# Performance work log

Hardware: AMD Instinct MI355X
Metric: run time of the kernel (lower is better)

Reference implementation:

```python
import jax, jax.numpy as jnp
import numpy as np

HID = 1024
PRED_LEN = 96


def lstm_cell(x, h, c, Wih, Whh, bih, bhh):
    # PyTorch LSTMCell: gates ordered i, f, g, o
    gates = x @ Wih.T + h @ Whh.T + bih + bhh
    i, f, g, o = jnp.split(gates, 4, axis=-1)
    c_new = jax.nn.sigmoid(f) * c + jax.nn.sigmoid(i) * jnp.tanh(g)
    h_new = jax.nn.sigmoid(o) * jnp.tanh(c_new)
    return h_new, c_new


def time_enc(idx, embs):
    # sum of 4 embedding lookups -> [..., time_encode_dim]
    return sum(e[idx[..., k]] for k, e in enumerate(embs))


def setup_inputs() -> dict:
    key = jax.random.key(0)
    ks = jax.random.split(key, 32)
    B, T, IN, OUT, H, TE = 256, 128, 7, 7, HID, 3
    d = {}
    d["x"] = jax.random.normal(ks[0], (B, T, IN), jnp.float32)
    d["y"] = jax.random.normal(ks[1], (B, PRED_LEN, OUT), jnp.float32)
    d["x_time_encode"] = jax.random.randint(ks[2], (B, T, 4), 0, 7)
    d["y_time_encode"] = jax.random.randint(ks[3], (B, PRED_LEN, 4), 0, 7)
    sizes = (12, 31, 24, 7)
    for i, n in enumerate(sizes):
        d[f"emb{i}"] = jax.random.normal(ks[4 + i], (n, TE), jnp.float32)
    ins = (IN + TE, H, H)
    s = float(1.0 / np.sqrt(H))
    for l in range(3):
        d[f"Wih{l}"] = jax.random.uniform(ks[8 + 4 * l], (4 * H, ins[l]), jnp.float32, -s, s)
        d[f"Whh{l}"] = jax.random.uniform(ks[9 + 4 * l], (4 * H, H), jnp.float32, -s, s)
        d[f"bih{l}"] = jax.random.uniform(ks[10 + 4 * l], (4 * H,), jnp.float32, -s, s)
        d[f"bhh{l}"] = jax.random.uniform(ks[11 + 4 * l], (4 * H,), jnp.float32, -s, s)
    d["fcW"] = jax.random.uniform(ks[20], (OUT, H), jnp.float32, -s, s)
    d["fcb"] = jax.random.uniform(ks[21], (OUT,), jnp.float32, -s, s)
    return d


def reference(x, y, x_time_encode, y_time_encode, emb0, emb1, emb2, emb3,
              Wih0, Whh0, bih0, bhh0, Wih1, Whh1, bih1, bhh1,
              Wih2, Whh2, bih2, bhh2, fcW, fcb):
    embs = (emb0, emb1, emb2, emb3)
    layers = ((Wih0, Whh0, bih0, bhh0),
              (Wih1, Whh1, bih1, bhh1),
              (Wih2, Whh2, bih2, bhh2))
    B = x.shape[0]
    H = Whh0.shape[1]

    # encode: concat time embedding, run stacked LSTM over time (dropout_rate=0 -> no-op)
    xin = jnp.concatenate([x, time_enc(x_time_encode, embs)], axis=-1)  # [B,T,in+te]
    h0 = tuple(jnp.zeros((B, H), x.dtype) for _ in range(3))

    def run_layers(hs, cs, inp):
        nh, nc = [], []
        for l, (Wih, Whh, bih, bhh) in enumerate(layers):
            h, c = lstm_cell(inp, hs[l], cs[l], Wih, Whh, bih, bhh)
            nh.append(h)
            nc.append(c)
            inp = h
        return tuple(nh), tuple(nc)

    def enc_step(carry, xt):
        hs, cs = carry
        hs, cs = run_layers(hs, cs, xt)
        return (hs, cs), None

    (hs, cs), _ = jax.lax.scan(enc_step, (h0, h0), xin.swapaxes(0, 1))

    y0 = hs[-1] @ fcW.T + fcb  # [B, out]

    def dec_step(carry, te_idx):
        hs, cs, y_prev = carry
        inp = jnp.concatenate([y_prev, time_enc(te_idx, embs)], axis=-1)
        hs, cs = run_layers(hs, cs, inp)
        yt = hs[-1] @ fcW.T + fcb
        return (hs, cs, yt), yt

    _, ys = jax.lax.scan(dec_step, (hs, cs, y0),
                         y_time_encode[:, :PRED_LEN - 1].swapaxes(0, 1))
    # [B, predict_len, out]
    return jnp.concatenate([y0[:, None], ys.swapaxes(0, 1)], axis=1)
```

## Files before the change

kernel.cpp:

```cpp
#include <hip/hip_runtime.h>

#define HID   1024
#define BATCH 256
#define TSEQ  128
#define PRED  96
#define IND   7
#define OUTD  7
#define SK    10

typedef __attribute__((ext_vector_type(8))) _Float16 f16x8;
typedef __attribute__((ext_vector_type(4))) float    f32x4;

#define BM   64
#define BN   64
#define GSTR 68

__device__ __forceinline__ float sigmoidf_fast(float x) {
  return 1.0f / (1.0f + __expf(-x));
}
__device__ __forceinline__ float tanhf_fast(float x) {
  float ax = fabsf(x);
  float e  = __expf(-2.0f * ax);
  float r  = (1.0f - e) / (1.0f + e);
  return copysignf(r, x);
}

__device__ __forceinline__ void async_cp16(const void* g, void* l) {
  __builtin_amdgcn_global_load_lds(
      (const __attribute__((address_space(1))) void*)g,
      (__attribute__((address_space(3))) void*)l, 16, 0, 0);
}

#define WBAR(N) asm volatile("s_waitcnt vmcnt(" #N ")\n\ts_barrier" ::: "memory")
#define BARO()  asm volatile("s_barrier" ::: "memory")

__global__ __launch_bounds__(256) void prep_kernel(
    const float* __restrict__ Wih0, const float* __restrict__ Whh0,
    const float* __restrict__ bih0, const float* __restrict__ bhh0,
    const float* __restrict__ Wih1, const float* __restrict__ Whh1,
    const float* __restrict__ bih1, const float* __restrict__ bhh1,
    const float* __restrict__ Wih2, const float* __restrict__ Whh2,
    const float* __restrict__ bih2, const float* __restrict__ bhh2,
    _Float16* __restrict__ B0, _Float16* __restrict__ B1, _Float16* __restrict__ B2,
    float* __restrict__ W0p, float* __restrict__ biasP)
{
  size_t e = (size_t)blockIdx.x * 256 + threadIdx.x;
  const size_t S0 = (size_t)4096 * 1024;
  const size_t S1 = (size_t)4096 * 2048;
  if (e < S0) {
    int n = (int)(e >> 10), k = (int)(e & 1023);
    int nb = n >> 6, gate = (n >> 4) & 3, u = n & 15;
    int r = gate * 1024 + nb * 16 + u;
    B0[e] = (_Float16)Whh0[(size_t)r * 1024 + k];
  } else if (e < S0 + S1) {
    size_t q = e - S0;
    int n = (int)(q >> 11), k = (int)(q & 2047);
    int nb = n >> 6, gate = (n >> 4) & 3, u = n & 15;
    int r = gate * 1024 + nb * 16 + u;
    float v = (k < 1024) ? Wih1[(size_t)r * 1024 + k]
                         : Whh1[(size_t)r * 1024 + (k - 1024)];
    B1[q] = (_Float16)v;
  } else if (e < S0 + 2 * S1) {
    size_t q = e - S0 - S1;
    int n = (int)(q >> 11), k = (int)(q & 2047);
    int nb = n >> 6, gate = (n >> 4) & 3, u = n & 15;
    int r = gate * 1024 + nb * 16 + u;
    float v = (k < 1024) ? Wih2[(size_t)r * 1024 + k]
                         : Whh2[(size_t)r * 1024 + (k - 1024)];
    B2[q] = (_Float16)v;
  } else if (e < S0 + 2 * S1 + 40960) {
    int q = (int)(e - S0 - 2 * S1);
    int n = q / 10, k = q - n * 10;
    int nb = n >> 6, gate = (n >> 4) & 3, u = n & 15;
    int r = gate * 1024 + nb * 16 + u;
    W0p[q] = Wih0[(size_t)r * 10 + k];
  } else if (e < S0 + 2 * S1 + 40960 + 12288) {
    int q = (int)(e - S0 - 2 * S1 - 40960);
    int l = q >> 12, n = q & 4095;
    int nb = n >> 6, gate = (n >> 4) & 3, u = n & 15;
    int r = gate * 1024 + nb * 16 + u;
    const float* bi = (l == 0) ? bih0 : (l == 1) ? bih1 : bih2;
    const float* bh = (l == 0) ? bhh0 : (l == 1) ? bhh1 : bhh2;
    biasP[q] = bi[r] + bh[r];
  }
}

__global__ __launch_bounds__(256) void lstm_wave(
    int d,
    _Float16* __restrict__ h0p0, _Float16* __restrict__ h0p1,
    _Float16* __restrict__ h1p0, _Float16* __restrict__ h1p1,
    _Float16* __restrict__ h2p0, _Float16* __restrict__ h2p1,
    const _Float16* __restrict__ B0g, const _Float16* __restrict__ B1g,
    const _Float16* __restrict__ B2g,
    const float* __restrict__ biasP, const float* __restrict__ W0p,
    float* __restrict__ c0, float* __restrict__ c1, float* __restrict__ c2,
    const float* __restrict__ x, const int* __restrict__ xte,
    const float* __restrict__ e0, const float* __restrict__ e1,
    const float* __restrict__ e2, const float* __restrict__ e3)
{
  __shared__ __align__(16) char smem[32768];
  __shared__ float SmallIn[BM * SK];
  __shared__ float W0s[BN * 11];

  const int layer = blockIdx.y >> 2;
  const int mb = blockIdx.y & 3, nb = blockIdx.x;
  const int t = d - layer;
  if (t < 0 || t >= TSEQ) return;
  const int p = d & 1;

  const _Float16 *A1, *A2; _Float16* ho; const _Float16* Bm;
  const float* bias; float* cst; int Kdim;
  if (layer == 0) {
    A1 = p ? h0p1 : h0p0; A2 = A1;              ho = p ? h0p0 : h0p1;
    Bm = B0g; bias = biasP;        cst = c0; Kdim = 1024;
  } else if (layer == 1) {
    A1 = p ? h0p1 : h0p0; A2 = p ? h1p1 : h1p0; ho = p ? h1p0 : h1p1;
    Bm = B1g; bias = biasP + 4096; cst = c1; Kdim = 2048;
  } else {
    A1 = p ? h1p1 : h1p0; A2 = p ? h2p1 : h2p0; ho = p ? h2p0 : h2p1;
    Bm = B2g; bias = biasP + 8192; cst = c2; Kdim = 2048;
  }
  const int Mbase = mb * BM;
  const int tid = threadIdx.x;

  if (layer == 0 && tid < BM) {
    int Mg = Mbase + tid;
    float v[SK];
    const float* xp = x + ((size_t)Mg * TSEQ + t) * IND;
#pragma unroll
    for (int i = 0; i < IND; ++i) v[i] = xp[i];
    const int* ip = xte + ((size_t)Mg * TSEQ + t) * 4;
    int i0 = ip[0], i1 = ip[1], i2 = ip[2], i3 = ip[3];
#pragma unroll
    for (int dd = 0; dd < 3; ++dd)
      v[IND + dd] = e0[i0 * 3 + dd] + e1[i1 * 3 + dd] + e2[i2 * 3 + dd] + e3[i3 * 3 + dd];
#pragma unroll
    for (int i = 0; i < SK; ++i) SmallIn[tid * SK + i] = v[i];
    const float* wp = W0p + (size_t)(nb * BN + tid) * SK;
#pragma unroll
    for (int i = 0; i < SK; ++i) W0s[tid * 11 + i] = wp[i];
  }

  _Float16* As = (_Float16*)smem;
  _Float16* Bs = (_Float16*)(smem + 16384);

  const int w = tid >> 6, lane = tid & 63;
  const int quad = lane >> 4, l16 = lane & 15;
  const int dr = lane >> 4, ds = lane & 15;

  size_t a_goff[4], b_goff[4];
  int lds_off[4];
#pragma unroll
  for (int i = 0; i < 4; ++i) {
    int lrow = w * 16 + i * 4 + dr;
    int sg = ds ^ (i * 4 + dr);
    a_goff[i] = (size_t)(Mbase + lrow) * (HID * 2) + (size_t)sg * 16;
    b_goff[i] = (size_t)(nb * BN + lrow) * ((size_t)Kdim * 2) + (size_t)sg * 16;
    lds_off[i] = lrow * 256 + ds * 16;
  }

  f32x4 acc[4] = {};

  for (int kk = 0; kk < Kdim; kk += 128) {
    const char* Abase = (kk < 1024)
        ? ((const char*)A1 + (size_t)kk * 2)
        : ((const char*)A2 + (size_t)(kk - 1024) * 2);
    const char* Bbase = (const char*)Bm + (size_t)kk * 2;
#pragma unroll
    for (int i = 0; i < 4; ++i) {
      async_cp16(Abase + a_goff[i], smem + lds_off[i]);
      async_cp16(Bbase + b_goff[i], smem + 16384 + lds_off[i]);
    }
    __syncthreads();
#pragma unroll
    for (int ks = 0; ks < 4; ++ks) {
      int segq = (ks * 4 + quad) ^ l16;
      f16x8 bf = *reinterpret_cast<const f16x8*>(Bs + (w * 16 + l16) * 128 + segq * 8);
#pragma unroll
      for (int mt = 0; mt < 4; ++mt) {
        f16x8 af = *reinterpret_cast<const f16x8*>(As + (mt * 16 + l16) * 128 + segq * 8);
        acc[mt] = __builtin_amdgcn_mfma_f32_16x16x32_f16(af, bf, acc[mt], 0, 0, 0);
      }
    }
    __syncthreads();
  }

  float* Gs = (float*)smem;
#pragma unroll
  for (int mt = 0; mt < 4; ++mt) {
    int row = mt * 16 + quad * 4;
    int col = w * 16 + l16;
#pragma unroll
    for (int r = 0; r < 4; ++r)
      Gs[(row + r) * GSTR + col] = acc[mt][r];
  }
  __syncthreads();

#pragma unroll
  for (int i = 0; i < 4; ++i) {
    int m = (tid >> 4) + i * 16;
    int u = tid & 15;
    float gi = Gs[m * GSTR + u];
    float gf = Gs[m * GSTR + 16 + u];
    float gg = Gs[m * GSTR + 32 + u];
    float go = Gs[m * GSTR + 48 + u];
    int nbase = nb * BN;
    gi += bias[nbase + u];
    gf += bias[nbase + 16 + u];
    gg += bias[nbase + 32 + u];
    go += bias[nbase + 48 + u];
    if (layer == 0) {
#pragma unroll
      for (int k = 0; k < SK; ++k) {
        float sv = SmallIn[m * SK + k];
        gi += sv * W0s[u * 11 + k];
        gf += sv * W0s[(16 + u) * 11 + k];
        gg += sv * W0s[(32 + u) * 11 + k];
        go += sv * W0s[(48 + u) * 11 + k];
      }
    }
    size_t cidx = (size_t)(Mbase + m) * HID + (size_t)nb * 16 + u;
    float cold = cst[cidx];
    float cn = sigmoidf_fast(gf) * cold + sigmoidf_fast(gi) * tanhf_fast(gg);
    float hn = sigmoidf_fast(go) * tanhf_fast(cn);
    cst[cidx] = cn;
    ho[cidx] = (_Float16)hn;
  }
}

template<int KCH, int MODE>
__global__ __launch_bounds__(256) void lstm_pipe(
    int s,
    const _Float16* __restrict__ A1, const _Float16* __restrict__ A2,
    const _Float16* __restrict__ Bm, const float* __restrict__ biasL,
    const float* __restrict__ W0p,
    float* __restrict__ cst, _Float16* __restrict__ hout,
    float* __restrict__ out, const int* __restrict__ yte,
    const float* __restrict__ e0, const float* __restrict__ e1,
    const float* __restrict__ e2, const float* __restrict__ e3,
    const float* __restrict__ fcW, const float* __restrict__ fcb)
{
  __shared__ __align__(16) char smem[3 * 16384];
  __shared__ float SmallIn[BM * SK];
  __shared__ float W0s[BN * 11];

  const int tid = threadIdx.x;
  const int nb = blockIdx.x, mb = blockIdx.y;
  const int Mbase = mb * BM;

  if (MODE == 1 && tid < BM) {
    int Mg = Mbase + tid;
    float v[SK];
    const float* yp = out + (size_t)Mg * (PRED * OUTD) + s * OUTD;
#pragma unroll
    for (int i = 0; i < OUTD; ++i) v[i] = yp[i];
    const int* ip = yte + ((size_t)Mg * PRED + s) * 4;
    int i0 = ip[0], i1 = ip[1], i2 = ip[2], i3 = ip[3];
#pragma unroll
    for (int dd = 0; dd < 3; ++dd)
      v[IND + dd] = e0[i0 * 3 + dd] + e1[i1 * 3 + dd] + e2[i2 * 3 + dd] + e3[i3 * 3 + dd];
#pragma unroll
    for (int i = 0; i < SK; ++i) SmallIn[tid * SK + i] = v[i];
    const float* wp = W0p + (size_t)(nb * BN + tid) * SK;
#pragma unroll
    for (int i = 0; i < SK; ++i) W0s[tid * 11 + i] = wp[i];
  }

  const int w = tid >> 6, lane = tid & 63;
  const int quad = lane >> 4, l16 = lane & 15;
  const int dr = lane >> 3, ds = lane & 7;

  size_t a_goff[2], b_goff[2];
  int lds_off[2];
#pragma unroll
  for (int i = 0; i < 2; ++i) {
    int lrow = w * 16 + i * 8 + dr;
    int sg = ds ^ dr;
    a_goff[i] = (size_t)(Mbase + lrow) * (HID * 2) + (size_t)sg * 16;
    b_goff[i] = (size_t)(nb * BN + lrow) * ((size_t)KCH * 128) + (size_t)sg * 16;
    lds_off[i] = lrow * 128 + ds * 16;
  }

  f32x4 acc[4] = {};

  __syncthreads();

#define ISSUE(c) do { \
    const char* Ab_ = (KCH == 16 || (c) < 16) \
        ? ((const char*)A1 + (size_t)(c) * 128) \
        : ((const char*)A2 + (size_t)((c) - 16) * 128); \
    const char* Bb_ = (const char*)Bm + (size_t)(c) * 128; \
    char* Lb_ = smem + ((c) % 3) * 16384; \
    _Pragma("unroll") \
    for (int i_ = 0; i_ < 2; ++i_) { \
      async_cp16(Ab_ + a_goff[i_], Lb_ + lds_off[i_]); \
      async_cp16(Bb_ + b_goff[i_], Lb_ + 8192 + lds_off[i_]); \
    } } while (0)

  ISSUE(0);
  ISSUE(1);
#pragma unroll
  for (int c = 0; c < KCH; ++c) {
    if (c + 2 < KCH) { ISSUE(c + 2); WBAR(8); }
    else if (c + 2 == KCH) { WBAR(4); }
    else { WBAR(0); }
    {
      const _Float16* As = (const _Float16*)(smem + (c % 3) * 16384);
      const _Float16* Bs = As + 4096;
#pragma unroll
      for (int ks = 0; ks < 2; ++ks) {
        int g = ks * 4 + quad;
        int sp = g ^ (l16 & 7);
        f16x8 bf = *reinterpret_cast<const f16x8*>(Bs + (w * 16 + l16) * 64 + sp * 8);
#pragma unroll
        for (int mt = 0; mt < 4; ++mt) {
          f16x8 af = *reinterpret_cast<const f16x8*>(As + (mt * 16 + l16) * 64 + sp * 8);
          acc[mt] = __builtin_amdgcn_mfma_f32_16x16x32_f16(af, bf, acc[mt], 0, 0, 0);
        }
      }
    }
    BARO();
  }
#undef ISSUE

  __syncthreads();
  float* Gs = (float*)smem;
#pragma unroll
  for (int mt = 0; mt < 4; ++mt) {
    int row = mt * 16 + quad * 4;
    int col = w * 16 + l16;
#pragma unroll
    for (int r = 0; r < 4; ++r)
      Gs[(row + r) * GSTR + col] = acc[mt][r];
  }
  __syncthreads();

  float w7[OUTD];
  if (MODE == 3) {
#pragma unroll
    for (int o = 0; o < OUTD; ++o)
      w7[o] = fcW[(size_t)o * HID + nb * 16 + (tid & 15)];
  }

#pragma unroll
  for (int i = 0; i < 4; ++i) {
    int m = (tid >> 4) + i * 16;
    int u = tid & 15;
    float gi = Gs[m * GSTR + u];
    float gf = Gs[m * GSTR + 16 + u];
    float gg = Gs[m * GSTR + 32 + u];
    float go = Gs[m * GSTR + 48 + u];
    int nbase = nb * BN;
    gi += biasL[nbase + u];
    gf += biasL[nbase + 16 + u];
    gg += biasL[nbase + 32 + u];
    go += biasL[nbase + 48 + u];
    if (MODE == 1) {
#pragma unroll
      for (int k = 0; k < SK; ++k) {
        float sv = SmallIn[m * SK + k];
        gi += sv * W0s[u * 11 + k];
        gf += sv * W0s[(16 + u) * 11 + k];
        gg += sv * W0s[(32 + u) * 11 + k];
        go += sv * W0s[(48 + u) * 11 + k];
      }
    }
    size_t cidx = (size_t)(Mbase + m) * HID + (size_t)nb * 16 + u;
    float cold = cst[cidx];
    float cn = sigmoidf_fast(gf) * cold + sigmoidf_fast(gi) * tanhf_fast(gg);
    float hn = sigmoidf_fast(go) * tanhf_fast(cn);
    cst[cidx] = cn;
    hout[cidx] = (_Float16)hn;

    if (MODE == 3) {
#pragma unroll
      for (int o = 0; o < OUTD; ++o) {
        float r = hn * w7[o];
        r += __shfl_xor(r, 1, 16);
        r += __shfl_xor(r, 2, 16);
        r += __shfl_xor(r, 4, 16);
        r += __shfl_xor(r, 8, 16);
        if (u == 0) {
          float val = r + ((nb == 0) ? fcb[o] : 0.0f);
          atomicAdd(&out[(size_t)(Mbase + m) * (PRED * OUTD) + (s + 1) * OUTD + o], val);
        }
      }
    }
  }
}

__global__ __launch_bounds__(256) void fc_kernel(
    const _Float16* __restrict__ h2, const float* __restrict__ fcW,
    const float* __restrict__ fcb, float* __restrict__ out)
{
  int wv = threadIdx.x >> 6, lane = threadIdx.x & 63;
  int row = blockIdx.x * 4 + wv;
  const _Float16* hp = h2 + (size_t)row * HID + lane * 16;
  float hv[16];
#pragma unroll
  for (int i = 0; i < 16; ++i) hv[i] = (float)hp[i];
  float acc[OUTD];
#pragma unroll
  for (int o = 0; o < OUTD; ++o) {
    const float* wp = fcW + (size_t)o * HID + lane * 16;
    float a = 0.f;
#pragma unroll
    for (int i = 0; i < 16; ++i) a += hv[i] * wp[i];
    acc[o] = a;
  }
#pragma unroll
  for (int o = 0; o < OUTD; ++o)
#pragma unroll
    for (int off = 32; off >= 1; off >>= 1)
      acc[o] += __shfl_xor(acc[o], off, 64);
  if (lane == 0) {
#pragma unroll
    for (int o = 0; o < OUTD; ++o)
      out[(size_t)row * (PRED * OUTD) + o] = acc[o] + fcb[o];
  }
}

extern "C" void kernel_launch(void* const* d_in, const int* in_sizes, int n_in,
                              void* d_out, int out_size, void* d_ws, size_t ws_size,
                              hipStream_t stream) {
  const float* x   = (const float*)d_in[0];
  const int*   xte = (const int*)d_in[2];
  const int*   yte = (const int*)d_in[3];
  const float* e0  = (const float*)d_in[4];
  const float* e1  = (const float*)d_in[5];
  const float* e2  = (const float*)d_in[6];
  const float* e3  = (const float*)d_in[7];
  const float* Wih0 = (const float*)d_in[8];
  const float* Whh0 = (const float*)d_in[9];
  const float* bih0 = (const float*)d_in[10];
  const float* bhh0 = (const float*)d_in[11];
  const float* Wih1 = (const float*)d_in[12];
  const float* Whh1 = (const float*)d_in[13];
  const float* bih1 = (const float*)d_in[14];
  const float* bhh1 = (const float*)d_in[15];
  const float* Wih2 = (const float*)d_in[16];
  const float* Whh2 = (const float*)d_in[17];
  const float* bih2 = (const float*)d_in[18];
  const float* bhh2 = (const float*)d_in[19];
  const float* fcW = (const float*)d_in[20];
  const float* fcb = (const float*)d_in[21];
  float* out = (float*)d_out;

  char* ws = (char*)d_ws;
  _Float16* B0   = (_Float16*)(ws);
  _Float16* B1   = (_Float16*)(ws + 8388608);
  _Float16* B2   = (_Float16*)(ws + 25165824);
  float*    W0p  = (float*)(ws + 41943040);
  float*    biasP= (float*)(ws + 42106880);
  char*     hp0  = ws + 42156032;
  float*    cbuf = (float*)(ws + 43728896);
  char*     hp1  = ws + 46874624;

  hipMemsetAsync(out, 0, (size_t)out_size * 4, stream);
  hipMemsetAsync(hp0, 0, 4718592, stream);
  hipMemsetAsync(hp1, 0, 1572864, stream);

  prep_kernel<<<82128, 256, 0, stream>>>(Wih0, Whh0, bih0, bhh0,
                                         Wih1, Whh1, bih1, bhh1,
                                         Wih2, Whh2, bih2, bhh2,
                                         B0, B1, B2, W0p, biasP);

  auto hb = [&](int l, int par) -> _Float16* {
    return (_Float16*)((par ? hp1 : hp0) + (size_t)l * 524288);
  };
  float* cl[3] = {cbuf, cbuf + 262144, cbuf + 524288};

  for (int d = 0; d < TSEQ + 2; ++d) {
    lstm_wave<<<dim3(64, 12), 256, 0, stream>>>(
        d, hb(0,0), hb(0,1), hb(1,0), hb(1,1), hb(2,0), hb(2,1),
        B0, B1, B2, biasP, W0p, cl[0], cl[1], cl[2],
        x, xte, e0, e1, e2, e3);
  }

  _Float16* hr0 = hb(0,0); _Float16* hw0 = hb(0,1);
  _Float16* hr1 = hb(1,1); _Float16* hw1 = hb(1,0);
  _Float16* hr2 = hb(2,0); _Float16* hw2 = hb(2,1);

  fc_kernel<<<64, 256, 0, stream>>>(hr2, fcW, fcb, out);

  dim3 dgrid(64, 4), blk(256);
  for (int s = 0; s < PRED - 1; ++s) {
    lstm_pipe<16, 1><<<dgrid, blk, 0, stream>>>(
        s, hr0, hr0, B0, biasP, W0p, cl[0], hw0,
        out, yte, e0, e1, e2, e3, fcW, fcb);
    lstm_pipe<32, 2><<<dgrid, blk, 0, stream>>>(
        s, hw0, hr1, B1, biasP + 4096, W0p, cl[1], hw1,
        out, yte, e0, e1, e2, e3, fcW, fcb);
    lstm_pipe<32, 3><<<dgrid, blk, 0, stream>>>(
        s, hw1, hr2, B2, biasP + 8192, W0p, cl[2], hw2,
        out, yte, e0, e1, e2, e3, fcW, fcb);
    _Float16* tmp;
    tmp = hr0; hr0 = hw0; hw0 = tmp;
    tmp = hr1; hr1 = hw1; hw1 = tmp;
    tmp = hr2; hr2 = hw2; hw2 = tmp;
  }
}
```

Measured before the change: 8.728 ms.

## Fuse decode loop into one persistent kernel with grid barriers and register cell state

Replaces the 285 per-layer decoder kernel launches with a single persistent kernel of 256 blocks that loops over all decode steps. Layers are separated by atomic grid-wide barriers. Cell state, biases and FC weights stay in registers across steps instead of being reloaded from global memory, and the K chunk is widened to 128 with a larger triple-buffered LDS pipeline. This targets launch overhead and repeated state traffic. In exchange it relies on all 256 blocks being co-resident for the spin barrier, and each barrier adds fence and polling cost.

```diff
diff --git a/kernel.cpp b/kernel.cpp
--- a/kernel.cpp
+++ b/kernel.cpp
@@ -33,6 +33,18 @@
 
 #define WBAR(N) asm volatile("s_waitcnt vmcnt(" #N ")\n\ts_barrier" ::: "memory")
 #define BARO()  asm volatile("s_barrier" ::: "memory")
+
+__device__ __forceinline__ void gridbar(unsigned* bar, unsigned tgt) {
+  __threadfence();
+  __syncthreads();
+  if (threadIdx.x == 0) {
+    __hip_atomic_fetch_add(bar, 1u, __ATOMIC_ACQ_REL, __HIP_MEMORY_SCOPE_AGENT);
+    while (__hip_atomic_load(bar, __ATOMIC_ACQUIRE, __HIP_MEMORY_SCOPE_AGENT) < tgt)
+      __builtin_amdgcn_s_sleep(8);
+  }
+  __syncthreads();
+  __threadfence();
+}
 
 __global__ __launch_bounds__(256) void prep_kernel(
     const float* __restrict__ Wih0, const float* __restrict__ Whh0,
@@ -228,103 +240,52 @@
   }
 }
 
-template<int KCH, int MODE>
-__global__ __launch_bounds__(256) void lstm_pipe(
-    int s,
-    const _Float16* __restrict__ A1, const _Float16* __restrict__ A2,
-    const _Float16* __restrict__ Bm, const float* __restrict__ biasL,
-    const float* __restrict__ W0p,
-    float* __restrict__ cst, _Float16* __restrict__ hout,
-    float* __restrict__ out, const int* __restrict__ yte,
-    const float* __restrict__ e0, const float* __restrict__ e1,
-    const float* __restrict__ e2, const float* __restrict__ e3,
-    const float* __restrict__ fcW, const float* __restrict__ fcb)
+template<int KC, int MODE>
+__device__ __forceinline__ void dec_layer(
+    const char* A1, const char* A2, const char* Bm,
+    const int* a_off, const int* b_off, const int* l_off,
+    char* smem, float* Gs, const float* SmallIn, const float* W0s,
+    const float* biasg, float* creg, _Float16* hout, float* out,
+    const float* w7, const float* fcadd, int s, int Mbase, int nb, int tid)
 {
-  __shared__ __align__(16) char smem[3 * 16384];
-  __shared__ float SmallIn[BM * SK];
-  __shared__ float W0s[BN * 11];
-
-  const int tid = threadIdx.x;
-  const int nb = blockIdx.x, mb = blockIdx.y;
-  const int Mbase = mb * BM;
-
-  if (MODE == 1 && tid < BM) {
-    int Mg = Mbase + tid;
-    float v[SK];
-    const float* yp = out + (size_t)Mg * (PRED * OUTD) + s * OUTD;
-#pragma unroll
-    for (int i = 0; i < OUTD; ++i) v[i] = yp[i];
-    const int* ip = yte + ((size_t)Mg * PRED + s) * 4;
-    int i0 = ip[0], i1 = ip[1], i2 = ip[2], i3 = ip[3];
-#pragma unroll
-    for (int dd = 0; dd < 3; ++dd)
-      v[IND + dd] = e0[i0 * 3 + dd] + e1[i1 * 3 + dd] + e2[i2 * 3 + dd] + e3[i3 * 3 + dd];
-#pragma unroll
-    for (int i = 0; i < SK; ++i) SmallIn[tid * SK + i] = v[i];
-    const float* wp = W0p + (size_t)(nb * BN + tid) * SK;
-#pragma unroll
-    for (int i = 0; i < SK; ++i) W0s[tid * 11 + i] = wp[i];
-  }
-
   const int w = tid >> 6, lane = tid & 63;
   const int quad = lane >> 4, l16 = lane & 15;
-  const int dr = lane >> 3, ds = lane & 7;
-
-  size_t a_goff[2], b_goff[2];
-  int lds_off[2];
-#pragma unroll
-  for (int i = 0; i < 2; ++i) {
-    int lrow = w * 16 + i * 8 + dr;
-    int sg = ds ^ dr;
-    a_goff[i] = (size_t)(Mbase + lrow) * (HID * 2) + (size_t)sg * 16;
-    b_goff[i] = (size_t)(nb * BN + lrow) * ((size_t)KCH * 128) + (size_t)sg * 16;
-    lds_off[i] = lrow * 128 + ds * 16;
-  }
-
   f32x4 acc[4] = {};
 
-  __syncthreads();
-
-#define ISSUE(c) do { \
-    const char* Ab_ = (KCH == 16 || (c) < 16) \
-        ? ((const char*)A1 + (size_t)(c) * 128) \
-        : ((const char*)A2 + (size_t)((c) - 16) * 128); \
-    const char* Bb_ = (const char*)Bm + (size_t)(c) * 128; \
-    char* Lb_ = smem + ((c) % 3) * 16384; \
+#define DISSUE(c) do { \
+    const char* Ab_ = (KC == 8 || (c) < 8) ? (A1 + (size_t)(c) * 256) \
+                                           : (A2 + (size_t)((c) - 8) * 256); \
+    const char* Bb_ = Bm + (size_t)(c) * 256; \
+    char* Lb_ = smem + ((c) % 3) * 32768; \
     _Pragma("unroll") \
-    for (int i_ = 0; i_ < 2; ++i_) { \
-      async_cp16(Ab_ + a_goff[i_], Lb_ + lds_off[i_]); \
-      async_cp16(Bb_ + b_goff[i_], Lb_ + 8192 + lds_off[i_]); \
+    for (int i_ = 0; i_ < 4; ++i_) { \
+      async_cp16(Ab_ + a_off[i_], Lb_ + l_off[i_]); \
+      async_cp16(Bb_ + b_off[i_], Lb_ + 16384 + l_off[i_]); \
     } } while (0)
 
-  ISSUE(0);
-  ISSUE(1);
-#pragma unroll
-  for (int c = 0; c < KCH; ++c) {
-    if (c + 2 < KCH) { ISSUE(c + 2); WBAR(8); }
-    else if (c + 2 == KCH) { WBAR(4); }
-    else { WBAR(0); }
-    {
-      const _Float16* As = (const _Float16*)(smem + (c % 3) * 16384);
-      const _Float16* Bs = As + 4096;
-#pragma unroll
-      for (int ks = 0; ks < 2; ++ks) {
-        int g = ks * 4 + quad;
-        int sp = g ^ (l16 & 7);
-        f16x8 bf = *reinterpret_cast<const f16x8*>(Bs + (w * 16 + l16) * 64 + sp * 8);
-#pragma unroll
-        for (int mt = 0; mt < 4; ++mt) {
-          f16x8 af = *reinterpret_cast<const f16x8*>(As + (mt * 16 + l16) * 64 + sp * 8);
-          acc[mt] = __builtin_amdgcn_mfma_f32_16x16x32_f16(af, bf, acc[mt], 0, 0, 0);
-        }
+  DISSUE(0);
+  DISSUE(1);
+#pragma unroll
+  for (int c = 0; c < KC; ++c) {
+    if (c + 2 < KC)       { DISSUE(c + 2); WBAR(16); }
+    else if (c + 2 == KC) { WBAR(8); }
+    else                  { WBAR(0); }
+    const _Float16* As = (const _Float16*)(smem + (c % 3) * 32768);
+    const _Float16* Bs = As + 8192;
+#pragma unroll
+    for (int ks = 0; ks < 4; ++ks) {
+      int sq = (ks * 4 + quad) ^ l16;
+      f16x8 bf = *reinterpret_cast<const f16x8*>(Bs + (w * 16 + l16) * 128 + sq * 8);
+#pragma unroll
+      for (int mt = 0; mt < 4; ++mt) {
+        f16x8 af = *reinterpret_cast<const f16x8*>(As + (mt * 16 + l16) * 128 + sq * 8);
+        acc[mt] = __builtin_amdgcn_mfma_f32_16x16x32_f16(af, bf, acc[mt], 0, 0, 0);
       }
     }
     BARO();
   }
-#undef ISSUE
-
-  __syncthreads();
-  float* Gs = (float*)smem;
+#undef DISSUE
+
 #pragma unroll
   for (int mt = 0; mt < 4; ++mt) {
     int row = mt * 16 + quad * 4;
@@ -335,26 +296,14 @@
   }
   __syncthreads();
 
-  float w7[OUTD];
-  if (MODE == 3) {
-#pragma unroll
-    for (int o = 0; o < OUTD; ++o)
-      w7[o] = fcW[(size_t)o * HID + nb * 16 + (tid & 15)];
-  }
-
 #pragma unroll
   for (int i = 0; i < 4; ++i) {
     int m = (tid >> 4) + i * 16;
     int u = tid & 15;
-    float gi = Gs[m * GSTR + u];
-    float gf = Gs[m * GSTR + 16 + u];
-    float gg = Gs[m * GSTR + 32 + u];
-    float go = Gs[m * GSTR + 48 + u];
-    int nbase = nb * BN;
-    gi += biasL[nbase + u];
-    gf += biasL[nbase + 16 + u];
-    gg += biasL[nbase + 32 + u];
-    go += biasL[nbase + 48 + u];
+    float gi = Gs[m * GSTR + u]      + biasg[0];
+    float gf = Gs[m * GSTR + 16 + u] + biasg[1];
+    float gg = Gs[m * GSTR + 32 + u] + biasg[2];
+    float go = Gs[m * GSTR + 48 + u] + biasg[3];
     if (MODE == 1) {
 #pragma unroll
       for (int k = 0; k < SK; ++k) {
@@ -365,13 +314,10 @@
         go += sv * W0s[(48 + u) * 11 + k];
       }
     }
-    size_t cidx = (size_t)(Mbase + m) * HID + (size_t)nb * 16 + u;
-    float cold = cst[cidx];
-    float cn = sigmoidf_fast(gf) * cold + sigmoidf_fast(gi) * tanhf_fast(gg);
+    float cn = sigmoidf_fast(gf) * creg[i] + sigmoidf_fast(gi) * tanhf_fast(gg);
     float hn = sigmoidf_fast(go) * tanhf_fast(cn);
-    cst[cidx] = cn;
-    hout[cidx] = (_Float16)hn;
-
+    creg[i] = cn;
+    hout[(size_t)(Mbase + m) * HID + (size_t)nb * 16 + u] = (_Float16)hn;
     if (MODE == 3) {
 #pragma unroll
       for (int o = 0; o < OUTD; ++o) {
@@ -380,12 +326,118 @@
         r += __shfl_xor(r, 2, 16);
         r += __shfl_xor(r, 4, 16);
         r += __shfl_xor(r, 8, 16);
-        if (u == 0) {
-          float val = r + ((nb == 0) ? fcb[o] : 0.0f);
-          atomicAdd(&out[(size_t)(Mbase + m) * (PRED * OUTD) + (s + 1) * OUTD + o], val);
-        }
+        if (u == 0)
+          atomicAdd(&out[(size_t)(Mbase + m) * (PRED * OUTD) + (s + 1) * OUTD + o],
+                    r + fcadd[o]);
       }
     }
+  }
+}
+
+__global__ __launch_bounds__(256, 1) void lstm_dec(
+    _Float16* __restrict__ h0a, _Float16* __restrict__ h0b,
+    _Float16* __restrict__ h1a, _Float16* __restrict__ h1b,
+    _Float16* __restrict__ h2a, _Float16* __restrict__ h2b,
+    const _Float16* __restrict__ B0g, const _Float16* __restrict__ B1g,
+    const _Float16* __restrict__ B2g,
+    const float* __restrict__ biasP, const float* __restrict__ W0p,
+    const float* __restrict__ cbuf,
+    float* __restrict__ out, const int* __restrict__ yte,
+    const float* __restrict__ e0, const float* __restrict__ e1,
+    const float* __restrict__ e2, const float* __restrict__ e3,
+    const float* __restrict__ fcW, const float* __restrict__ fcb,
+    unsigned* __restrict__ bar)
+{
+  __shared__ __align__(16) char smem[3 * 32768];
+  __shared__ float Gs[BM * GSTR];
+  __shared__ float SmallIn[BM * SK];
+  __shared__ float W0s[BN * 11];
+
+  const int tid = threadIdx.x;
+  const int nb = blockIdx.x & 63, mb = blockIdx.x >> 6;
+  const int Mbase = mb * BM;
+  const int w = tid >> 6, lane = tid & 63;
+  const int dr = lane >> 4, ds = lane & 15;
+
+  int a_off[4], b1_off[4], b2_off[4], l_off[4];
+#pragma unroll
+  for (int i = 0; i < 4; ++i) {
+    int lrow = w * 16 + i * 4 + dr;
+    int sg = ds ^ (i * 4 + dr);
+    a_off[i]  = (Mbase + lrow) * 2048 + sg * 16;
+    b1_off[i] = (nb * 64 + lrow) * 2048 + sg * 16;
+    b2_off[i] = (nb * 64 + lrow) * 4096 + sg * 16;
+    l_off[i]  = lrow * 256 + ds * 16;
+  }
+
+  if (tid < BN) {
+    const float* wp = W0p + (size_t)(nb * BN + tid) * SK;
+#pragma unroll
+    for (int i = 0; i < SK; ++i) W0s[tid * 11 + i] = wp[i];
+  }
+
+  const int u = tid & 15;
+  float biasr[3][4];
+#pragma unroll
+  for (int l = 0; l < 3; ++l)
+#pragma unroll
+    for (int g = 0; g < 4; ++g)
+      biasr[l][g] = biasP[l * 4096 + nb * 64 + g * 16 + u];
+
+  float creg[3][4];
+#pragma unroll
+  for (int l = 0; l < 3; ++l)
+#pragma unroll
+    for (int i = 0; i < 4; ++i) {
+      int m = (tid >> 4) + i * 16;
+      creg[l][i] = cbuf[(size_t)l * 262144 + (size_t)(Mbase + m) * HID + nb * 16 + u];
+    }
+
+  float w7[OUTD], fcadd[OUTD];
+#pragma unroll
+  for (int o = 0; o < OUTD; ++o) {
+    w7[o] = fcW[(size_t)o * HID + nb * 16 + u];
+    fcadd[o] = (nb == 0) ? fcb[o] : 0.0f;
+  }
+
+  _Float16* h0[2] = {h0a, h0b};
+  _Float16* h1[2] = {h1a, h1b};
+  _Float16* h2[2] = {h2a, h2b};
+  int p0 = 0, p1 = 1, p2 = 0;
+  unsigned bc = 0;
+
+  for (int s = 0; s < PRED - 1; ++s) {
+    if (tid < BM) {
+      int Mg = Mbase + tid;
+      float v[SK];
+      const float* yp = out + (size_t)Mg * (PRED * OUTD) + s * OUTD;
+#pragma unroll
+      for (int i = 0; i < OUTD; ++i) v[i] = yp[i];
+      const int* ip = yte + ((size_t)Mg * PRED + s) * 4;
+      int i0 = ip[0], i1 = ip[1], i2 = ip[2], i3 = ip[3];
+#pragma unroll
+      for (int dd = 0; dd < 3; ++dd)
+        v[IND + dd] = e0[i0 * 3 + dd] + e1[i1 * 3 + dd] + e2[i2 * 3 + dd] + e3[i3 * 3 + dd];
+#pragma unroll
+      for (int i = 0; i < SK; ++i) SmallIn[tid * SK + i] = v[i];
+    }
+
+    dec_layer<8, 1>((const char*)h0[p0], (const char*)h0[p0], (const char*)B0g,
+                    a_off, b1_off, l_off, smem, Gs, SmallIn, W0s,
+                    biasr[0], creg[0], h0[1 - p0], out, w7, fcadd, s, Mbase, nb, tid);
+    gridbar(bar, ++bc * 256);
+
+    dec_layer<16, 2>((const char*)h0[1 - p0], (const char*)h1[p1], (const char*)B1g,
+                     a_off, b2_off, l_off, smem, Gs, SmallIn, W0s,
+                     biasr[1], creg[1], h1[1 - p1], out, w7, fcadd, s, Mbase, nb, tid);
+    gridbar(bar, ++bc * 256);
+
+    dec_layer<16, 3>((const char*)h1[1 - p1], (const char*)h2[p2], (const char*)B2g,
+                     a_off, b2_off, l_off, smem, Gs, SmallIn, W0s,
+                     biasr[2], creg[2], h2[1 - p2], out, w7, fcadd, s, Mbase, nb, tid);
+    gridbar(bar, ++bc * 256);
+
+    p0 ^= 1; p1 ^= 1; p2 ^= 1;
   }
 }
 
@@ -455,10 +507,12 @@
   char*     hp0  = ws + 42156032;
   float*    cbuf = (float*)(ws + 43728896);
   char*     hp1  = ws + 46874624;
+  unsigned* bar  = (unsigned*)(ws + 48447488);
 
   hipMemsetAsync(out, 0, (size_t)out_size * 4, stream);
   hipMemsetAsync(hp0, 0, 4718592, stream);
   hipMemsetAsync(hp1, 0, 1572864, stream);
+  hipMemsetAsync(bar, 0, 4, stream);
 
   prep_kernel<<<82128, 256, 0, stream>>>(Wih0, Whh0, bih0, bhh0,
                                          Wih1, Whh1, bih1, bhh1,
@@ -477,26 +531,10 @@
         x, xte, e0, e1, e2, e3);
   }
 
-  _Float16* hr0 = hb(0,0); _Float16* hw0 = hb(0,1);
-  _Float16* hr1 = hb(1,1); _Float16* hw1 = hb(1,0);
-  _Float16* hr2 = hb(2,0); _Float16* hw2 = hb(2,1);
-
-  fc_kernel<<<64, 256, 0, stream>>>(hr2, fcW, fcb, out);
-
-  dim3 dgrid(64, 4), blk(256);
-  for (int s = 0; s < PRED - 1; ++s) {
-    lstm_pipe<16, 1><<<dgrid, blk, 0, stream>>>(
-        s, hr0, hr0, B0, biasP, W0p, cl[0], hw0,
-        out, yte, e0, e1, e2, e3, fcW, fcb);
-    lstm_pipe<32, 2><<<dgrid, blk, 0, stream>>>(
-        s, hw0, hr1, B1, biasP + 4096, W0p, cl[1], hw1,
-        out, yte, e0, e1, e2, e3, fcW, fcb);
-    lstm_pipe<32, 3><<<dgrid, blk, 0, stream>>>(
-        s, hw1, hr2, B2, biasP + 8192, W0p, cl[2], hw2,
-        out, yte, e0, e1, e2, e3, fcW, fcb);
-    _Float16* tmp;
-    tmp = hr0; hr0 = hw0; hw0 = tmp;
-    tmp = hr1; hr1 = hw1; hw1 = tmp;
-    tmp = hr2; hr2 = hw2; hw2 = tmp;
-  }
-}
+  fc_kernel<<<64, 256, 0, stream>>>(hb(2,0), fcW, fcb, out);
+
+  lstm_dec<<<256, 256, 0, stream>>>(
+      hb(0,0), hb(0,1), hb(1,0), hb(1,1), hb(2,0), hb(2,1),
+      B0, B1, B2, biasP, W0p, cbuf,
+      out, yte, e0, e1, e2, e3, fcW, fcb, bar);
+}
```

After: 21.06 ms. +141.2%, slower.
